# Optimization experiments

Measured on AMD Instinct MI355X. Metric: run time of the kernel, lower is better.

The kernel has to match this reference:

```python
import jax, jax.numpy as jnp
import numpy as np

N_DRUG, N_CELL, N_GENE = 1000, 1000, 6000
N = N_DRUG + N_CELL + N_GENE
H1, H2, H3, HEADS = 256, 128, 128, 4
E = 160000
B = 10000


def _gat_layer(x, src, dst, ea, W, b, a_s, a_d, We, a_e, bias, heads, ch):
    # PyG GATConv (single shared lin for src/dst), edge_dim=1, concat=True, slope=0.2
    n = x.shape[0]
    xw = (x @ W + b).reshape(n, heads, ch)                     # [N,H,C]
    a_src = jnp.einsum('nhc,hc->nh', xw, a_s)                  # [N,H]
    a_dst = jnp.einsum('nhc,hc->nh', xw, a_d)
    eemb = (ea[:, None] @ We).reshape(-1, heads, ch)           # [E',H,C]
    a_edge = jnp.einsum('ehc,hc->eh', eemb, a_e)               # [E',H]
    alpha = jax.nn.leaky_relu(a_src[src] + a_dst[dst] + a_edge, 0.2)
    # segment softmax over destination node (flow source->target)
    m = jax.ops.segment_max(alpha, dst, num_segments=n)
    ex = jnp.exp(alpha - m[dst])
    denom = jax.ops.segment_sum(ex, dst, num_segments=n)
    att = ex / (denom[dst] + 1e-16)                            # [E',H]
    out = jax.ops.segment_sum(xw[src] * att[:, :, None], dst, num_segments=n)
    return out.reshape(n, heads * ch) + bias, att


def _graph_norm(x, gamma, beta, mean_scale, eps=1e-5):
    mu = x.mean(0)
    out = x - mean_scale * mu
    var = (out * out).mean(0)
    return gamma * out / jnp.sqrt(var + eps) + beta


def _attn_mat(src, dst, att, n):
    # original sets every edge entry to the scalar mean of all attention weights
    return jnp.zeros((n, n), dtype=att.dtype).at[src, dst].set(att.mean())


def setup_inputs() -> dict:
    key = jax.random.key(0)
    ks = jax.random.split(key, 40)
    s = 0.1
    inp = {
        'drug': jax.random.normal(ks[0], (N_DRUG, N_DRUG), jnp.float32),
        'cell': jax.random.normal(ks[1], (N_CELL, N_CELL), jnp.float32),
        'gene': jax.random.normal(ks[2], (N_GENE, N_GENE), jnp.float32),
        'edge_attr': jax.random.uniform(ks[3], (E,), jnp.float32),
        'edge_index': jax.random.randint(ks[4], (2, E), 0, N),
        'idx_drug': jax.random.randint(ks[5], (B,), 0, N_DRUG),
        'idx_cell': jax.random.randint(ks[6], (B,), 0, N),
        # type-specific input projections
        'W_drug': jax.random.normal(ks[7], (N_DRUG, H1)) * s, 'b_drug': jnp.zeros((H1,)),
        'W_cell': jax.random.normal(ks[8], (N_CELL, H1)) * s, 'b_cell': jnp.zeros((H1,)),
        'W_gene': jax.random.normal(ks[9], (N_GENE, H1)) * s, 'b_gene': jnp.zeros((H1,)),
        # gat1
        'W1': jax.random.normal(ks[10], (H1, HEADS * H2)) * s, 'b1': jnp.zeros((HEADS * H2,)),
        'att_src1': jax.random.normal(ks[11], (HEADS, H2)) * s,
        'att_dst1': jax.random.normal(ks[12], (HEADS, H2)) * s,
        'We1': jax.random.normal(ks[13], (1, HEADS * H2)) * s,
        'att_e1': jax.random.normal(ks[14], (HEADS, H2)) * s,
        'bias1': jnp.zeros((HEADS * H2,)),
        'g1': jnp.ones((HEADS * H2,)), 'be1': jnp.zeros((HEADS * H2,)), 'ms1': jnp.ones((HEADS * H2,)),
        # gat2
        'W2': jax.random.normal(ks[15], (HEADS * H2, HEADS * H3)) * s, 'b2': jnp.zeros((HEADS * H3,)),
        'att_src2': jax.random.normal(ks[16], (HEADS, H3)) * s,
        'att_dst2': jax.random.normal(ks[17], (HEADS, H3)) * s,
        'We2': jax.random.normal(ks[18], (1, HEADS * H3)) * s,
        'att_e2': jax.random.normal(ks[19], (HEADS, H3)) * s,
        'bias2': jnp.zeros((HEADS * H3,)),
        'g2': jnp.ones((HEADS * H3,)), 'be2': jnp.zeros((HEADS * H3,)), 'ms2': jnp.ones((HEADS * H3,)),
        # head
        'Wout': jax.random.normal(ks[20], (2 * HEADS * H3, 1)) * s, 'bout': jnp.zeros((1,)),
    }
    return inp


def reference(drug, cell, gene, edge_attr, edge_index, idx_drug, idx_cell,
              W_drug, b_drug, W_cell, b_cell, W_gene, b_gene,
              W1, b1, att_src1, att_dst1, We1, att_e1, bias1, g1, be1, ms1,
              W2, b2, att_src2, att_dst2, We2, att_e2, bias2, g2, be2, ms2,
              Wout, bout):
    x = jnp.concatenate([drug @ W_drug + b_drug,
                         cell @ W_cell + b_cell,
                         gene @ W_gene + b_gene], axis=0)       # [N,H1]
    # GATConv adds self-loops with edge_attr filled by the mean edge attribute
    loop = jnp.arange(N)
    src = jnp.concatenate([edge_index[0], loop])
    dst = jnp.concatenate([edge_index[1], loop])
    ea = jnp.concatenate([edge_attr, jnp.full((N,), edge_attr.mean(), edge_attr.dtype)])

    x, att1 = _gat_layer(x, src, dst, ea, W1, b1, att_src1, att_dst1, We1, att_e1, bias1, HEADS, H2)
    all_att = _attn_mat(src, dst, att1, N)
    x = jax.nn.relu(_graph_norm(x, g1, be1, ms1))               # dropout = identity (eval)

    x, att2 = _gat_layer(x, src, dst, ea, W2, b2, att_src2, att_dst2, We2, att_e2, bias2, HEADS, H3)
    all_att = all_att + _attn_mat(src, dst, att2, N)
    x = jax.nn.relu(_graph_norm(x, g2, be2, ms2))

    x = jnp.concatenate([x[idx_drug], x[idx_cell]], axis=1) @ Wout + bout  # [B,1]
    return x, all_att
```

## Files before the change

kernel.cpp:

```cpp
#include <hip/hip_runtime.h>
#include <math.h>

#define NDRUG 1000
#define NCELL 1000
#define NGENE 6000
#define NNODE 8000
#define H1 256
#define HD  512
#define E0  160000
#define ET  168000
#define BSZ 10000
#define GKP 6016
#define ZSPLIT 8
#define ZCH 768

typedef __attribute__((ext_vector_type(8))) short bf16x8;
typedef __attribute__((ext_vector_type(4))) float f32x4;

__device__ inline unsigned short f2bf(float f)
{
    unsigned u = __float_as_uint(f);
    u += 0x7fffu + ((u >> 16) & 1u);
    return (unsigned short)(u >> 16);
}
__device__ inline float bf2f(unsigned short h)
{
    return __uint_as_float(((unsigned)h) << 16);
}

__global__ void cvt_pad2_dc_kernel(const float* __restrict__ drug, unsigned short* dh, unsigned short* dl,
                                   const float* __restrict__ cell, unsigned short* ch, unsigned short* cl)
{
    const float* in;
    unsigned short *hi, *lo;
    long u0;
    if (blockIdx.x < 512) { in = drug; hi = dh; lo = dl; u0 = (long)blockIdx.x * 256 + threadIdx.x; }
    else                  { in = cell; hi = ch; lo = cl; u0 = (long)(blockIdx.x - 512) * 256 + threadIdx.x; }
    const long total = (long)1024 * 1024 / 8;
    for (long u = u0; u < total; u += 512 * 256) {
        long row = u / 128; int kc = (int)(u % 128);
        unsigned short oh[8], ol[8];
        if (row < 1000 && kc * 8 < 1000) {
            const float* p = in + row * 1000 + kc * 8;
            float4 a = *(const float4*)p, b = *(const float4*)(p + 4);
            float v[8] = {a.x, a.y, a.z, a.w, b.x, b.y, b.z, b.w};
            #pragma unroll
            for (int i = 0; i < 8; ++i) {
                unsigned short h = f2bf(v[i]);
                oh[i] = h;
                ol[i] = f2bf(v[i] - bf2f(h));
            }
        } else {
            #pragma unroll
            for (int i = 0; i < 8; ++i) { oh[i] = 0; ol[i] = 0; }
        }
        *(uint4*)(hi + u * 8) = *(const uint4*)oh;
        *(uint4*)(lo + u * 8) = *(const uint4*)ol;
    }
}


struct TC5 {
    const float* W[5];
    unsigned short* Wh[5];
    unsigned short* Wl[5];
    int K[5]; int N[5]; int Kp[5]; int gx[5];
    int start[6];
};

__global__ __launch_bounds__(256) void transpose_cvt2_batch(TC5 d)
{
    int bid = blockIdx.x;
    int idx = 0;
    #pragma unroll
    for (int i = 1; i < 5; ++i) if (bid >= d.start[i]) idx = i;
    int local = bid - d.start[idx];
    int gx = d.gx[idx];
    int K = d.K[idx], N = d.N[idx], Kp = d.Kp[idx];
    const float* W = d.W[idx];
    unsigned short* Wh = d.Wh[idx];
    unsigned short* Wl = d.Wl[idx];
    __shared__ float t[32][33];
    int kb = (local % gx) * 32, nb = (local / gx) * 32;
    int tx = threadIdx.x & 31, ty = threadIdx.x >> 5;
    #pragma unroll
    for (int i = 0; i < 32; i += 8) {
        int k = kb + ty + i;
        t[ty + i][tx] = (k < K) ? W[(long)k * N + nb + tx] : 0.f;
    }
    __syncthreads();
    #pragma unroll
    for (int i = 0; i < 32; i += 8) {
        int n = nb + ty + i;
        float v = t[tx][ty + i];
        unsigned short h = f2bf(v);
        Wh[(long)n * Kp + kb + tx] = h;
        Wl[(long)n * Kp + kb + tx] = f2bf(v - bf2f(h));
    }
}

template<int OUTBF>
__global__ __launch_bounds__(256) void gemm_mfma2(const unsigned short* __restrict__ Ah,
                                                  const unsigned short* __restrict__ Al,
                                                  const unsigned short* __restrict__ Bh,
                                                  const unsigned short* __restrict__ Bl,
                                                  const float* __restrict__ bias,
                                                  float* __restrict__ Cf,
                                                  unsigned short* __restrict__ Cbh,
                                                  unsigned short* __restrict__ Cbl,
                                                  unsigned short* __restrict__ Cx,
                                                  int M, int Kp, int N)
{
    __shared__ unsigned short AsH[64 * 64];
    __shared__ unsigned short AsL[64 * 64];
    __shared__ unsigned short BsH[64 * 64];
    __shared__ unsigned short BsL[64 * 64];
    char* AsH8 = (char*)AsH; char* AsL8 = (char*)AsL;
    char* BsH8 = (char*)BsH; char* BsL8 = (char*)BsL;
    int tid = threadIdx.x;
    int w = tid >> 6, l = tid & 63;
    int wr = w >> 1, wc = w & 1;
    int g = l >> 4, r16 = l & 15;
    int row0 = blockIdx.y * 64, col0 = blockIdx.x * 64;
    int srow = tid >> 3, skc = tid & 7;
    int B0 = srow * 128 + skc * 16;       int P0 = B0 ^ ((srow & 7) << 4);
    int r1 = srow + 32;                   int B1 = r1 * 128 + skc * 16;
    int P1 = B1 ^ ((r1 & 7) << 4);
    f32x4 acc[2][2] = {};
    for (int k0 = 0; k0 < Kp; k0 += 64) {
        long a0 = (long)(row0 + srow) * Kp + k0 + skc * 8;
        long a1 = (long)(row0 + srow + 32) * Kp + k0 + skc * 8;
        long b0 = (long)(col0 + srow) * Kp + k0 + skc * 8;
        long b1 = (long)(col0 + srow + 32) * Kp + k0 + skc * 8;
        uint4 ah0 = *(const uint4*)(Ah + a0); uint4 ah1 = *(const uint4*)(Ah + a1);
        uint4 al0 = *(const uint4*)(Al + a0); uint4 al1 = *(const uint4*)(Al + a1);
        uint4 bh0 = *(const uint4*)(Bh + b0); uint4 bh1 = *(const uint4*)(Bh + b1);
        uint4 bl0 = *(const uint4*)(Bl + b0); uint4 bl1 = *(const uint4*)(Bl + b1);
        __syncthreads();
        *(uint4*)(AsH8 + P0) = ah0; *(uint4*)(AsH8 + P1) = ah1;
        *(uint4*)(AsL8 + P0) = al0; *(uint4*)(AsL8 + P1) = al1;
        *(uint4*)(BsH8 + P0) = bh0; *(uint4*)(BsH8 + P1) = bh1;
        *(uint4*)(BsL8 + P0) = bl0; *(uint4*)(BsL8 + P1) = bl1;
        __syncthreads();
        #pragma unroll
        for (int kk = 0; kk < 2; ++kk) {
            bf16x8 afh[2], afl[2], bfh[2], bfl[2];
            #pragma unroll
            for (int m = 0; m < 2; ++m) {
                int row = wr * 32 + m * 16 + r16;
                int Bb = (row * 128 + kk * 64 + g * 16) ^ ((row & 7) << 4);
                afh[m] = *(const bf16x8*)(AsH8 + Bb);
                afl[m] = *(const bf16x8*)(AsL8 + Bb);
            }
            #pragma unroll
            for (int n = 0; n < 2; ++n) {
                int row = wc * 32 + n * 16 + r16;
                int Bb = (row * 128 + kk * 64 + g * 16) ^ ((row & 7) << 4);
                bfh[n] = *(const bf16x8*)(BsH8 + Bb);
                bfl[n] = *(const bf16x8*)(BsL8 + Bb);
            }
            #pragma unroll
            for (int m = 0; m < 2; ++m)
                #pragma unroll
                for (int n = 0; n < 2; ++n) {
                    acc[m][n] = __builtin_amdgcn_mfma_f32_16x16x32_bf16(afh[m], bfh[n], acc[m][n], 0, 0, 0);
                    acc[m][n] = __builtin_amdgcn_mfma_f32_16x16x32_bf16(afh[m], bfl[n], acc[m][n], 0, 0, 0);
                    acc[m][n] = __builtin_amdgcn_mfma_f32_16x16x32_bf16(afl[m], bfh[n], acc[m][n], 0, 0, 0);
                }
        }
    }
    #pragma unroll
    for (int m = 0; m < 2; ++m) {
        #pragma unroll
        for (int n = 0; n < 2; ++n) {
            #pragma unroll
            for (int r = 0; r < 4; ++r) {
                int rowg = row0 + wr * 32 + m * 16 + g * 4 + r;
                int colg = col0 + wc * 32 + n * 16 + r16;
                if (rowg < M) {
                    float v = acc[m][n][r] + bias[colg];
                    if (OUTBF) {
                        unsigned short h = f2bf(v);
                        Cbh[(long)rowg * N + colg] = h;
                        Cbl[(long)rowg * N + colg] = f2bf(v - bf2f(h));
                    } else {
                        Cf[(long)rowg * N + colg] = v;
                        Cx[(long)rowg * N + colg] = f2bf(v);
                    }
                }
            }
        }
    }
}

__global__ __launch_bounds__(256) void gemm_gene_f32(const float* __restrict__ A,
                                                     const unsigned short* __restrict__ Bh,
                                                     const unsigned short* __restrict__ Bl,
                                                     float* __restrict__ part)
{
    __shared__ char lds[65536];
    int tid = threadIdx.x;
    int w = tid >> 6, l = tid & 63;
    int wr = w >> 1, wc = w & 1;
    int g = l >> 4, r16 = l & 15;
    int pid = blockIdx.x;
    int L = (pid & 7) * 94 + (pid >> 3);
    int xb = L & 1;
    int yb = (L >> 1) % 47;
    int z  = L / 94;
    int row0 = yb * 128, col0 = xb * 128;
    int kbeg = z * ZCH;
    int kend = kbeg + ZCH; if (kend > GKP) kend = GKP;
    int niter = (kend - kbeg) >> 5;
    int arow = tid >> 1, akp = (tid & 1) * 16;
    int t_ar = (arow + (arow >> 2)) & 3;
    int s0 = akp >> 3;
    int wo0 = arow * 64 + ((s0 ^ t_ar) << 4);
    int wo1 = arow * 64 + (((s0 + 1) ^ t_ar) << 4);
    int tA = (r16 + (r16 >> 2)) & 3;
    int soA = (g ^ tA) << 4;
    int gr = row0 + arow;
    const float* arowp = A + (long)gr * NGENE;
    const unsigned short* bhp = Bh + (long)(col0 + arow) * GKP;
    const unsigned short* blp = Bl + (long)(col0 + arow) * GKP;
    bool arok = (gr < NGENE);
    f32x4 acc[4][4] = {};

    float av[16];
    uint4 rbh0, rbh1, rbl0, rbl1;
    {
        int gk = kbeg + akp;
        #pragma unroll
        for (int j = 0; j < 16; j += 4) {
            float4 v = (arok && gk + j < NGENE) ? *(const float4*)(arowp + gk + j)
                                                : make_float4(0.f, 0.f, 0.f, 0.f);
            av[j] = v.x; av[j + 1] = v.y; av[j + 2] = v.z; av[j + 3] = v.w;
        }
        rbh0 = *(const uint4*)(bhp + gk); rbh1 = *(const uint4*)(bhp + gk + 8);
        rbl0 = *(const uint4*)(blp + gk); rbl1 = *(const uint4*)(blp + gk + 8);
    }
    {
        unsigned short ah[16], alr[16];
        #pragma unroll
        for (int j = 0; j < 16; ++j) {
            unsigned u = __float_as_uint(av[j]);
            ah[j] = (unsigned short)(u >> 16);
            alr[j] = f2bf(av[j] - __uint_as_float(u & 0xffff0000u));
        }
        char* AsH = lds; char* AsL = lds + 8192;
        char* BsH = lds + 16384; char* BsL = lds + 24576;
        *(uint4*)(AsH + wo0) = *(const uint4*)&ah[0];
        *(uint4*)(AsH + wo1) = *(const uint4*)&ah[8];
        *(uint4*)(AsL + wo0) = *(const uint4*)&alr[0];
        *(uint4*)(AsL + wo1) = *(const uint4*)&alr[8];
        *(uint4*)(BsH + wo0) = rbh0; *(uint4*)(BsH + wo1) = rbh1;
        *(uint4*)(BsL + wo0) = rbl0; *(uint4*)(BsL + wo1) = rbl1;
    }
    __syncthreads();
    for (int i = 0; i < niter; ++i) {
        bool more = (i + 1 < niter);
        if (more) {
            int gk = kbeg + (i + 1) * 32 + akp;
            #pragma unroll
            for (int j = 0; j < 16; j += 4) {
                float4 v = (arok && gk + j < NGENE) ? *(const float4*)(arowp + gk + j)
                                                    : make_float4(0.f, 0.f, 0.f, 0.f);
                av[j] = v.x; av[j + 1] = v.y; av[j + 2] = v.z; av[j + 3] = v.w;
            }
            rbh0 = *(const uint4*)(bhp + gk); rbh1 = *(const uint4*)(bhp + gk + 8);
            rbl0 = *(const uint4*)(blp + gk); rbl1 = *(const uint4*)(blp + gk + 8);
        }
        {
            char* base = lds + (i & 1) * 32768;
            char* AsH = base; char* AsL = base + 8192;
            char* BsH = base + 16384; char* BsL = base + 24576;
            bf16x8 afh[4], afl[4], bfh[4], bfl[4];
            #pragma unroll
            for (int m = 0; m < 4; ++m) {
                int Bb = (wr * 64 + m * 16 + r16) * 64 + soA;
                afh[m] = *(const bf16x8*)(AsH + Bb);
                afl[m] = *(const bf16x8*)(AsL + Bb);
            }
            #pragma unroll
            for (int n = 0; n < 4; ++n) {
                int Bb = (wc * 64 + n * 16 + r16) * 64 + soA;
                bfh[n] = *(const bf16x8*)(BsH + Bb);
                bfl[n] = *(const bf16x8*)(BsL + Bb);
            }
            #pragma unroll
            for (int m = 0; m < 4; ++m)
                #pragma unroll
                for (int n = 0; n < 4; ++n) {
                    acc[m][n] = __builtin_amdgcn_mfma_f32_16x16x32_bf16(afh[m], bfh[n], acc[m][n], 0, 0, 0);
                    acc[m][n] = __builtin_amdgcn_mfma_f32_16x16x32_bf16(afh[m], bfl[n], acc[m][n], 0, 0, 0);
                    acc[m][n] = __builtin_amdgcn_mfma_f32_16x16x32_bf16(afl[m], bfh[n], acc[m][n], 0, 0, 0);
                }
        }
        if (more) {
            unsigned short ah[16], alr[16];
            #pragma unroll
            for (int j = 0; j < 16; ++j) {
                unsigned u = __float_as_uint(av[j]);
                ah[j] = (unsigned short)(u >> 16);
                alr[j] = f2bf(av[j] - __uint_as_float(u & 0xffff0000u));
            }
            char* base = lds + ((i + 1) & 1) * 32768;
            char* AsH = base; char* AsL = base + 8192;
            char* BsH = base + 16384; char* BsL = base + 24576;
            *(uint4*)(AsH + wo0) = *(const uint4*)&ah[0];
            *(uint4*)(AsH + wo1) = *(const uint4*)&ah[8];
            *(uint4*)(AsL + wo0) = *(const uint4*)&alr[0];
            *(uint4*)(AsL + wo1) = *(const uint4*)&alr[8];
            *(uint4*)(BsH + wo0) = rbh0; *(uint4*)(BsH + wo1) = rbh1;
            *(uint4*)(BsL + wo0) = rbl0; *(uint4*)(BsL + wo1) = rbl1;
        }
        __syncthreads();
    }
    #pragma unroll
    for (int m = 0; m < 4; ++m) {
        #pragma unroll
        for (int n = 0; n < 4; ++n) {
            #pragma unroll
            for (int r = 0; r < 4; ++r) {
                int rowg = row0 + wr * 64 + m * 16 + g * 4 + r;
                int colg = col0 + wc * 64 + n * 16 + r16;
                if (rowg < NGENE)
                    part[((long)z * NGENE + rowg) * H1 + colg] = acc[m][n][r];
            }
        }
    }
}

__global__ __launch_bounds__(256) void reduce_splitk_kernel(const float* __restrict__ part,
                                                            const float* __restrict__ bias,
                                                            unsigned short* __restrict__ xh,
                                                            unsigned short* __restrict__ xl)
{
    const long NEL = (long)NGENE * H1;
    long stride = (long)gridDim.x * blockDim.x;
    for (long q = (long)blockIdx.x * blockDim.x + threadIdx.x; q * 4 < NEL; q += stride) {
        long e = q * 4;
        float4 sv = *(const float4*)(part + e);
        #pragma unroll
        for (int z = 1; z < ZSPLIT; ++z) {
            float4 t = *(const float4*)(part + (long)z * NEL + e);
            sv.x += t.x; sv.y += t.y; sv.z += t.z; sv.w += t.w;
        }
        int col = (int)(e & (H1 - 1));
        float4 b = *(const float4*)(bias + col);
        float v[4] = {sv.x + b.x, sv.y + b.y, sv.z + b.z, sv.w + b.w};
        unsigned short oh[4], ol[4];
        #pragma unroll
        for (int i = 0; i < 4; ++i) {
            oh[i] = f2bf(v[i]);
            ol[i] = f2bf(v[i] - bf2f(oh[i]));
        }
        long o = (long)(NDRUG + NCELL) * H1 + e;
        *(uint2*)(xh + o) = *(const uint2*)oh;
        *(uint2*)(xl + o) = *(const uint2*)ol;
    }
}

__global__ void init1_kernel(float* m, int* deg, float* colstats, float* scal)
{
    int i = blockIdx.x * 256 + threadIdx.x;
    if (i < NNODE * 4) m[i] = -3.402823466e38f;
    if (i < NNODE) deg[i] = 0;
    if (i < 1024) colstats[i] = 0.f;
    if (i < 8) scal[i] = 0.f;
}

__global__ void init2_kernel(float* m, float* colstats)
{
    int i = blockIdx.x * 256 + threadIdx.x;
    if (i < NNODE * 4) m[i] = -3.402823466e38f;
    if (i < 1024) colstats[i] = 0.f;
}

__global__ __launch_bounds__(512) void small_pre_kernel(const float* __restrict__ eattr, float* scal,
                                                        const float* We1, const float* ae1,
                                                        const float* We2, const float* ae2, float* ce)
{
    if (blockIdx.x < 64) {
        float s = 0.f;
        for (int i = blockIdx.x * 512 + threadIdx.x; i < E0; i += 64 * 512)
            s += eattr[i];
        for (int off = 32; off; off >>= 1) s += __shfl_down(s, off);
        if ((threadIdx.x & 63) == 0) atomicAdd(&scal[0], s);
    } else {
        __shared__ float sm[512];
        int t = threadIdx.x;
        sm[t] = We1[t] * ae1[t];
        __syncthreads();
        if (t < 4) { float s = 0.f; for (int c = 0; c < 128; ++c) s += sm[t * 128 + c]; ce[t] = s; }
        __syncthreads();
        sm[t] = We2[t] * ae2[t];
        __syncthreads();
        if (t < 4) { float s = 0.f; for (int c = 0; c < 128; ++c) s += sm[t * 128 + c]; ce[4 + t] = s; }
    }
}

__global__ void deg_kernel(const int* __restrict__ ei, int* __restrict__ deg)
{
    int e = blockIdx.x * blockDim.x + threadIdx.x;
    if (e >= ET) return;
    int d = (e < E0) ? ei[E0 + e] : (e - E0);
    atomicAdd(&deg[d], 1);
}

__global__ __launch_bounds__(1024) void scan_kernel(const int* __restrict__ deg,
                                                    int* __restrict__ row_start,
                                                    int* __restrict__ cursor)
{
    __shared__ int sm[1024];
    int t = threadIdx.x;
    int base = t * 8;
    int loc[8];
    int sum = 0;
    #pragma unroll
    for (int j = 0; j < 8; ++j) {
        int v = (base + j < NNODE) ? deg[base + j] : 0;
        loc[j] = sum; sum += v;
    }
    sm[t] = sum;
    __syncthreads();
    for (int off = 1; off < 1024; off <<= 1) {
        int v = (t >= off) ? sm[t - off] : 0;
        __syncthreads();
        sm[t] += v;
        __syncthreads();
    }
    int excl = sm[t] - sum;
    #pragma unroll
    for (int j = 0; j < 8; ++j) {
        int idx = base + j;
        if (idx < NNODE) { int v = excl + loc[j]; row_start[idx] = v; cursor[idx] = v; }
    }
    if (t == 1023) row_start[NNODE] = sm[1023];
}

__global__ void scatter_csr_kernel(const int* __restrict__ ei, int* __restrict__ cursor,
                                   int* __restrict__ csr_src, int* __restrict__ pos_of_e)
{
    int e = blockIdx.x * blockDim.x + threadIdx.x;
    if (e >= ET) return;
    int s, d;
    if (e < E0) { s = ei[e]; d = ei[E0 + e]; }
    else        { s = d = e - E0; }
    int pos = atomicAdd(&cursor[d], 1);
    csr_src[pos] = s;
    pos_of_e[e] = pos;
}

__global__ __launch_bounds__(256) void attn_coef_kernel(const float* __restrict__ xw,
                                                        const float* __restrict__ as,
                                                        const float* __restrict__ ad,
                                                        float* __restrict__ a_src,
                                                        float* __restrict__ a_dst)
{
    int n = blockIdx.x * 4 + (threadIdx.x >> 6);
    int l = threadIdx.x & 63;
    #pragma unroll
    for (int h = 0; h < 4; ++h) {
        float x1 = xw[(long)n * HD + h * 128 + l];
        float x2 = xw[(long)n * HD + h * 128 + 64 + l];
        float s = x1 * as[h * 128 + l] + x2 * as[h * 128 + 64 + l];
        float d = x1 * ad[h * 128 + l] + x2 * ad[h * 128 + 64 + l];
        for (int off = 32; off; off >>= 1) { s += __shfl_down(s, off); d += __shfl_down(d, off); }
        if (l == 0) { a_src[n * 4 + h] = s; a_dst[n * 4 + h] = d; }
    }
}

__device__ inline void atomicMaxF(float* addr, float v)
{
    if (v >= 0.f) atomicMax((int*)addr, __float_as_int(v));
    else          atomicMin((unsigned int*)addr, __float_as_uint(v));
}

__global__ void alpha_max_kernel(const int* __restrict__ ei, const float* __restrict__ eattr,
                                 const float* __restrict__ scal,
                                 const float* __restrict__ a_src, const float* __restrict__ a_dst,
                                 const float* __restrict__ ce,
                                 float* __restrict__ csr_alpha,
                                 const int* __restrict__ pos_of_e,
                                 float* __restrict__ m)
{
    int e = blockIdx.x * blockDim.x + threadIdx.x;
    if (e >= ET) return;
    int s, d; float a;
    if (e < E0) { s = ei[e]; d = ei[E0 + e]; a = eattr[e]; }
    else        { s = d = e - E0; a = scal[0] * (1.0f / E0); }
    float4 av;
    float* avp = (float*)&av;
    #pragma unroll
    for (int h = 0; h < 4; ++h) {
        float v = a_src[s * 4 + h] + a_dst[d * 4 + h] + a * ce[h];
        v = v > 0.f ? v : 0.2f * v;
        avp[h] = v;
        atomicMaxF(&m[d * 4 + h], v);
    }
    *(float4*)(csr_alpha + (long)pos_of_e[e] * 4) = av;
}

__global__ __launch_bounds__(256) void aggregate_kernel(const unsigned short* __restrict__ xwb,
                                                        const float* __restrict__ csr_alpha,
                                                        const float* __restrict__ m,
                                                        const int* __restrict__ rs,
                                                        const int* __restrict__ csr_src,
                                                        const float* __restrict__ bias,
                                                        float* __restrict__ out)
{
    int n = blockIdx.x;
    int h = threadIdx.x >> 6;
    int l = threadIdx.x & 63;
    float mnh = m[n * 4 + h];
    int i0 = rs[n], i1 = rs[n + 1];
    float den = 0.f;
    for (int i = i0 + l; i < i1; i += 64)
        den += expf(csr_alpha[(long)i * 4 + h] - mnh);
    for (int off = 32; off; off >>= 1) den += __shfl_down(den, off);
    den = __shfl(den, 0);
    float rden = 1.0f / (den + 1e-16f);
    float acc0 = 0.f, acc1 = 0.f;
    int i = i0;
    for (; i + 7 < i1; i += 8) {
        int      sv[8];
        float    av[8];
        unsigned xv[8];
        #pragma unroll
        for (int j = 0; j < 8; ++j) {
            sv[j] = csr_src[i + j];
            av[j] = csr_alpha[(long)(i + j) * 4 + h];
        }
        #pragma unroll
        for (int j = 0; j < 8; ++j)
            xv[j] = *(const unsigned*)(xwb + (long)sv[j] * HD + h * 128 + 2 * l);
        #pragma unroll
        for (int j = 0; j < 8; ++j) {
            float w = expf(av[j] - mnh);
            acc0 += w * bf2f((unsigned short)(xv[j] & 0xffffu));
            acc1 += w * bf2f((unsigned short)(xv[j] >> 16));
        }
    }
    for (; i < i1; ++i) {
        int s = csr_src[i];
        float w = expf(csr_alpha[(long)i * 4 + h] - mnh);
        unsigned x = *(const unsigned*)(xwb + (long)s * HD + h * 128 + 2 * l);
        acc0 += w * bf2f((unsigned short)(x & 0xffffu));
        acc1 += w * bf2f((unsigned short)(x >> 16));
    }
    float2 o;
    o.x = acc0 * rden + bias[h * 128 + 2 * l];
    o.y = acc1 * rden + bias[h * 128 + 2 * l + 1];
    *(float2*)(out + (long)n * HD + h * 128 + 2 * l) = o;
}

__global__ __launch_bounds__(256) void colstats_kernel(const float* __restrict__ x,
                                                       float* __restrict__ colsum,
                                                       float* __restrict__ colsumsq)
{
    int t = threadIdx.x, b = blockIdx.x;
    float s0 = 0.f, s1 = 0.f, q0 = 0.f, q1 = 0.f;
    for (int r = b * 125; r < (b + 1) * 125; ++r) {
        float v0 = x[(long)r * HD + t];
        float v1 = x[(long)r * HD + t + 256];
        s0 += v0; q0 += v0 * v0;
        s1 += v1; q1 += v1 * v1;
    }
    atomicAdd(&colsum[t], s0);
    atomicAdd(&colsum[t + 256], s1);
    atomicAdd(&colsumsq[t], q0);
    atomicAdd(&colsumsq[t + 256], q1);
}

__global__ void norm_kernel(float* __restrict__ x,
                            unsigned short* __restrict__ xbh, unsigned short* __restrict__ xbl,
                            const float* __restrict__ colsum,
                            const float* __restrict__ colsumsq,
                            const float* __restrict__ g, const float* __restrict__ be,
                            const float* __restrict__ ms)
{
    int stride = gridDim.x * blockDim.x;
    for (int idx = blockIdx.x * blockDim.x + threadIdx.x; idx < NNODE * HD; idx += stride) {
        int j = idx & 511;
        float mu  = colsum[j] * (1.0f / NNODE);
        float ex2 = colsumsq[j] * (1.0f / NNODE);
        float msj = ms[j];
        float var = ex2 - msj * (2.0f - msj) * mu * mu;
        float v = x[idx] - msj * mu;
        float y = g[j] * v / sqrtf(var + 1e-5f) + be[j];
        y = y > 0.f ? y : 0.f;
        x[idx] = y;
        unsigned short h = f2bf(y);
        xbh[idx] = h;
        xbl[idx] = f2bf(y - bf2f(h));
    }
}

__global__ __launch_bounds__(256) void head_kernel(const float* __restrict__ x2,
                                                   const int* __restrict__ idd,
                                                   const int* __restrict__ idc,
                                                   const float* __restrict__ Wout,
                                                   const float* __restrict__ bout,
                                                   float* __restrict__ out0)
{
    int w = threadIdx.x >> 6, l = threadIdx.x & 63;
    int b = blockIdx.x * 4 + w;
    if (b >= BSZ) return;
    int rd = idd[b], rc = idc[b];
    float s = 0.f;
    #pragma unroll
    for (int k = l; k < HD; k += 64)
        s += x2[(long)rd * HD + k] * Wout[k] + x2[(long)rc * HD + k] * Wout[HD + k];
    for (int off = 32; off; off >>= 1) s += __shfl_down(s, off);
    if (l == 0) out0[b] = s + bout[0];
}

__global__ void zero_f4_kernel(float4* __restrict__ p, long n4)
{
    long stride = (long)gridDim.x * blockDim.x;
    for (long i = (long)blockIdx.x * blockDim.x + threadIdx.x; i < n4; i += stride)
        p[i] = make_float4(0.f, 0.f, 0.f, 0.f);
}

__global__ void scatter_att_kernel(const int* __restrict__ ei, float* __restrict__ attm)
{
    int e = blockIdx.x * blockDim.x + threadIdx.x;
    if (e >= ET) return;
    int s, d;
    if (e < E0) { s = ei[e]; d = ei[E0 + e]; }
    else        { s = d = e - E0; }
    const float val = 2.0f * (float)NNODE / (float)ET;
    attm[(long)s * NNODE + d] = val;
}

extern "C" void kernel_launch(void* const* d_in, const int* in_sizes, int n_in,
                              void* d_out, int out_size, void* d_ws, size_t ws_size,
                              hipStream_t stream)
{
    const float* drug   = (const float*)d_in[0];
    const float* cell   = (const float*)d_in[1];
    const float* gene   = (const float*)d_in[2];
    const float* eattr  = (const float*)d_in[3];
    const int*   ei     = (const int*)d_in[4];
    const int*   idd    = (const int*)d_in[5];
    const int*   idc    = (const int*)d_in[6];
    const float* Wdrug  = (const float*)d_in[7];
    const float* bdrug  = (const float*)d_in[8];
    const float* Wcell  = (const float*)d_in[9];
    const float* bcell  = (const float*)d_in[10];
    const float* Wgene  = (const float*)d_in[11];
    const float* bgene  = (const float*)d_in[12];
    const float* W1     = (const float*)d_in[13];
    const float* b1     = (const float*)d_in[14];
    const float* as1    = (const float*)d_in[15];
    const float* ad1    = (const float*)d_in[16];
    const float* We1    = (const float*)d_in[17];
    const float* ae1    = (const float*)d_in[18];
    const float* bias1  = (const float*)d_in[19];
    const float* g1     = (const float*)d_in[20];
    const float* be1    = (const float*)d_in[21];
    const float* ms1    = (const float*)d_in[22];
    const float* W2     = (const float*)d_in[23];
    const float* b2     = (const float*)d_in[24];
    const float* as2    = (const float*)d_in[25];
    const float* ad2    = (const float*)d_in[26];
    const float* We2    = (const float*)d_in[27];
    const float* ae2    = (const float*)d_in[28];
    const float* bias2  = (const float*)d_in[29];
    const float* g2     = (const float*)d_in[30];
    const float* be2    = (const float*)d_in[31];
    const float* ms2    = (const float*)d_in[32];
    const float* Wout   = (const float*)d_in[33];
    const float* bout   = (const float*)d_in[34];

    float* out0 = (float*)d_out;
    float* attm = (float*)d_out + BSZ;

    float* ws     = (float*)d_ws;
    float* xw     = ws;
    float* outb   = xw + (long)NNODE * HD;
    float* csr_al = outb + (long)NNODE * HD;
    float* a_src  = csr_al + (long)ET * 4;
    float* a_dst  = a_src + NNODE * 4;
    float* mbuf   = a_dst + NNODE * 4;
    float* colsum = mbuf + NNODE * 4;
    float* colsq  = colsum + 512;
    float* ce     = colsq + 512;
    float* scal   = ce + 8;
    int* deg      = (int*)(scal + 8);
    int* rs       = deg + NNODE;
    int* cursor   = rs + NNODE + 4;
    int* csr_src  = cursor + NNODE;
    int* pos_of_e = csr_src + ET;
    unsigned short* p = (unsigned short*)(pos_of_e + ET);
    unsigned short* xwb    = p; p += (long)NNODE * HD;
    unsigned short* drug_h = p; p += (long)1024 * 1024;
    unsigned short* drug_l = p; p += (long)1024 * 1024;
    unsigned short* cell_h = p; p += (long)1024 * 1024;
    unsigned short* cell_l = p; p += (long)1024 * 1024;
    unsigned short* x0_h   = p; p += (long)NNODE * H1;
    unsigned short* x0_l   = p; p += (long)NNODE * H1;
    unsigned short* xb_h   = p; p += (long)NNODE * HD;
    unsigned short* xb_l   = p; p += (long)NNODE * HD;
    unsigned short* Wd_h   = p; p += 256 * 1024;
    unsigned short* Wd_l   = p; p += 256 * 1024;
    unsigned short* Wc_h   = p; p += 256 * 1024;
    unsigned short* Wc_l   = p; p += 256 * 1024;
    unsigned short* Wg_h   = p; p += 256 * GKP;
    unsigned short* Wg_l   = p; p += 256 * GKP;
    unsigned short* W1_h   = p; p += 512 * 256;
    unsigned short* W1_l   = p; p += 512 * 256;
    unsigned short* W2_h   = p; p += 512 * 512;
    unsigned short* W2_l   = p; p += 512 * 512;
    float* partsk = (float*)((((unsigned long long)p) + 15) & ~15ULL);

    dim3 blk256(256);
    int gE = (ET + 255) / 256;

    init1_kernel<<<125, blk256, 0, stream>>>(mbuf, deg, colsum, scal);
    deg_kernel<<<gE, blk256, 0, stream>>>(ei, deg);
    scan_kernel<<<1, 1024, 0, stream>>>(deg, rs, cursor);
    scatter_csr_kernel<<<gE, blk256, 0, stream>>>(ei, cursor, csr_src, pos_of_e);
    small_pre_kernel<<<65, 512, 0, stream>>>(eattr, scal, We1, ae1, We2, ae2, ce);

    cvt_pad2_dc_kernel<<<1024, blk256, 0, stream>>>(drug, drug_h, drug_l, cell, cell_h, cell_l);
    {
        TC5 d;
        d.W[0] = Wdrug; d.Wh[0] = Wd_h; d.Wl[0] = Wd_l; d.K[0] = NDRUG; d.N[0] = H1; d.Kp[0] = 1024; d.gx[0] = 32;
        d.W[1] = Wcell; d.Wh[1] = Wc_h; d.Wl[1] = Wc_l; d.K[1] = NCELL; d.N[1] = H1; d.Kp[1] = 1024; d.gx[1] = 32;
        d.W[2] = Wgene; d.Wh[2] = Wg_h; d.Wl[2] = Wg_l; d.K[2] = NGENE; d.N[2] = H1; d.Kp[2] = GKP;  d.gx[2] = 188;
        d.W[3] = W1;    d.Wh[3] = W1_h; d.Wl[3] = W1_l; d.K[3] = H1;    d.N[3] = HD; d.Kp[3] = H1;   d.gx[3] = 8;
        d.W[4] = W2;    d.Wh[4] = W2_h; d.Wl[4] = W2_l; d.K[4] = HD;    d.N[4] = HD; d.Kp[4] = HD;   d.gx[4] = 16;
        d.start[0] = 0;    d.start[1] = 256;  d.start[2] = 512;
        d.start[3] = 2016; d.start[4] = 2144; d.start[5] = 2400;
        transpose_cvt2_batch<<<2400, blk256, 0, stream>>>(d);
    }

    gemm_mfma2<1><<<dim3(H1 / 64, 16), blk256, 0, stream>>>(drug_h, drug_l, Wd_h, Wd_l, bdrug,
        nullptr, x0_h, x0_l, nullptr, NDRUG, 1024, H1);
    gemm_mfma2<1><<<dim3(H1 / 64, 16), blk256, 0, stream>>>(cell_h, cell_l, Wc_h, Wc_l, bcell,
        nullptr, x0_h + (long)NDRUG * H1, x0_l + (long)NDRUG * H1, nullptr, NCELL, 1024, H1);
    gemm_gene_f32<<<752, blk256, 0, stream>>>(gene, Wg_h, Wg_l, partsk);
    reduce_splitk_kernel<<<1500, blk256, 0, stream>>>(partsk, bgene, x0_h, x0_l);

    gemm_mfma2<0><<<dim3(HD / 64, NNODE / 64), blk256, 0, stream>>>(x0_h, x0_l, W1_h, W1_l, b1,
        xw, nullptr, nullptr, xwb, NNODE, H1, HD);
    attn_coef_kernel<<<NNODE / 4, blk256, 0, stream>>>(xw, as1, ad1, a_src, a_dst);
    alpha_max_kernel<<<gE, blk256, 0, stream>>>(ei, eattr, scal, a_src, a_dst, ce,
        csr_al, pos_of_e, mbuf);
    aggregate_kernel<<<NNODE, blk256, 0, stream>>>(xwb, csr_al, mbuf, rs, csr_src, bias1, outb);
    colstats_kernel<<<64, blk256, 0, stream>>>(outb, colsum, colsq);
    norm_kernel<<<2048, blk256, 0, stream>>>(outb, xb_h, xb_l, colsum, colsq, g1, be1, ms1);

    gemm_mfma2<0><<<dim3(HD / 64, NNODE / 64), blk256, 0, stream>>>(xb_h, xb_l, W2_h, W2_l, b2,
        xw, nullptr, nullptr, xwb, NNODE, HD, HD);
    attn_coef_kernel<<<NNODE / 4, blk256, 0, stream>>>(xw, as2, ad2, a_src, a_dst);
    init2_kernel<<<125, blk256, 0, stream>>>(mbuf, colsum);
    alpha_max_kernel<<<gE, blk256, 0, stream>>>(ei, eattr, scal, a_src, a_dst, ce + 4,
        csr_al, pos_of_e, mbuf);
    aggregate_kernel<<<NNODE, blk256, 0, stream>>>(xwb, csr_al, mbuf, rs, csr_src, bias2, outb);
    colstats_kernel<<<64, blk256, 0, stream>>>(outb, colsum, colsq);
    norm_kernel<<<2048, blk256, 0, stream>>>(outb, xb_h, xb_l, colsum, colsq, g2, be2, ms2);

    head_kernel<<<(BSZ + 3) / 4, blk256, 0, stream>>>(outb, idd, idc, Wout, bout, out0);
    zero_f4_kernel<<<2048, blk256, 0, stream>>>((float4*)attm, (long)NNODE * NNODE / 4);
    scatter_att_kernel<<<gE, blk256, 0, stream>>>(ei, attm);
}
```

Measured before the change: 576.2 us.

## Load gene GEMM MFMA fragments directly from global memory, dropping LDS staging

The split-K gene GEMM no longer stages A and B tiles through double-buffered shared memory. Each lane loads its own MFMA fragment rows straight from global memory, converting fp32 A to hi/lo bf16 in registers. This removes LDS writes, reads and the per-iteration barriers, and frees LDS so more blocks can share a CU. In exchange, each A and B element is fetched by several waves instead of once per block, which leans on L2/L1 caching. Each lane also does strided 32-byte loads rather than coalesced row loads, and the A hi/lo conversion is now repeated by every wave that reads the row.

```diff
diff --git a/kernel.cpp b/kernel.cpp
--- a/kernel.cpp
+++ b/kernel.cpp
@@ -58,7 +58,6 @@
         *(uint4*)(lo + u * 8) = *(const uint4*)ol;
     }
 }
-
 
 struct TC5 {
     const float* W[5];
@@ -193,12 +192,11 @@
     }
 }
 
-__global__ __launch_bounds__(256) void gemm_gene_f32(const float* __restrict__ A,
-                                                     const unsigned short* __restrict__ Bh,
-                                                     const unsigned short* __restrict__ Bl,
-                                                     float* __restrict__ part)
-{
-    __shared__ char lds[65536];
+__global__ __launch_bounds__(256) void gemm_gene_noLDS(const float* __restrict__ A,
+                                                       const unsigned short* __restrict__ Bh,
+                                                       const unsigned short* __restrict__ Bl,
+                                                       float* __restrict__ part)
+{
     int tid = threadIdx.x;
     int w = tid >> 6, l = tid & 63;
     int wr = w >> 1, wc = w & 1;
@@ -211,110 +209,60 @@
     int row0 = yb * 128, col0 = xb * 128;
     int kbeg = z * ZCH;
     int kend = kbeg + ZCH; if (kend > GKP) kend = GKP;
-    int niter = (kend - kbeg) >> 5;
-    int arow = tid >> 1, akp = (tid & 1) * 16;
-    int t_ar = (arow + (arow >> 2)) & 3;
-    int s0 = akp >> 3;
-    int wo0 = arow * 64 + ((s0 ^ t_ar) << 4);
-    int wo1 = arow * 64 + (((s0 + 1) ^ t_ar) << 4);
-    int tA = (r16 + (r16 >> 2)) & 3;
-    int soA = (g ^ tA) << 4;
-    int gr = row0 + arow;
-    const float* arowp = A + (long)gr * NGENE;
-    const unsigned short* bhp = Bh + (long)(col0 + arow) * GKP;
-    const unsigned short* blp = Bl + (long)(col0 + arow) * GKP;
-    bool arok = (gr < NGENE);
+    int koff = g * 8;
+    const float* arp[4];
+    bool arok[4];
+    #pragma unroll
+    for (int m = 0; m < 4; ++m) {
+        int r = row0 + wr * 64 + m * 16 + r16;
+        arok[m] = (r < NGENE);
+        arp[m] = A + (long)r * NGENE;
+    }
+    const unsigned short* bhp[4];
+    const unsigned short* blp[4];
+    #pragma unroll
+    for (int n = 0; n < 4; ++n) {
+        int c = col0 + wc * 64 + n * 16 + r16;
+        bhp[n] = Bh + (long)c * GKP;
+        blp[n] = Bl + (long)c * GKP;
+    }
     f32x4 acc[4][4] = {};
-
-    float av[16];
-    uint4 rbh0, rbh1, rbl0, rbl1;
-    {
-        int gk = kbeg + akp;
-        #pragma unroll
-        for (int j = 0; j < 16; j += 4) {
-            float4 v = (arok && gk + j < NGENE) ? *(const float4*)(arowp + gk + j)
-                                                : make_float4(0.f, 0.f, 0.f, 0.f);
-            av[j] = v.x; av[j + 1] = v.y; av[j + 2] = v.z; av[j + 3] = v.w;
-        }
-        rbh0 = *(const uint4*)(bhp + gk); rbh1 = *(const uint4*)(bhp + gk + 8);
-        rbl0 = *(const uint4*)(blp + gk); rbl1 = *(const uint4*)(blp + gk + 8);
-    }
-    {
-        unsigned short ah[16], alr[16];
-        #pragma unroll
-        for (int j = 0; j < 16; ++j) {
-            unsigned u = __float_as_uint(av[j]);
-            ah[j] = (unsigned short)(u >> 16);
-            alr[j] = f2bf(av[j] - __uint_as_float(u & 0xffff0000u));
-        }
-        char* AsH = lds; char* AsL = lds + 8192;
-        char* BsH = lds + 16384; char* BsL = lds + 24576;
-        *(uint4*)(AsH + wo0) = *(const uint4*)&ah[0];
-        *(uint4*)(AsH + wo1) = *(const uint4*)&ah[8];
-        *(uint4*)(AsL + wo0) = *(const uint4*)&alr[0];
-        *(uint4*)(AsL + wo1) = *(const uint4*)&alr[8];
-        *(uint4*)(BsH + wo0) = rbh0; *(uint4*)(BsH + wo1) = rbh1;
-        *(uint4*)(BsL + wo0) = rbl0; *(uint4*)(BsL + wo1) = rbl1;
-    }
-    __syncthreads();
-    for (int i = 0; i < niter; ++i) {
-        bool more = (i + 1 < niter);
-        if (more) {
-            int gk = kbeg + (i + 1) * 32 + akp;
-            #pragma unroll
-            for (int j = 0; j < 16; j += 4) {
-                float4 v = (arok && gk + j < NGENE) ? *(const float4*)(arowp + gk + j)
-                                                    : make_float4(0.f, 0.f, 0.f, 0.f);
-                av[j] = v.x; av[j + 1] = v.y; av[j + 2] = v.z; av[j + 3] = v.w;
+    #pragma unroll 2
+    for (int k0 = kbeg; k0 < kend; k0 += 32) {
+        int gk = k0 + koff;
+        bool kok = (gk + 8 <= NGENE);
+        bf16x8 afh[4], afl[4], bfh[4], bfl[4];
+        #pragma unroll
+        for (int m = 0; m < 4; ++m) {
+            float4 v0 = make_float4(0.f, 0.f, 0.f, 0.f), v1 = v0;
+            if (arok[m] && kok) {
+                v0 = *(const float4*)(arp[m] + gk);
+                v1 = *(const float4*)(arp[m] + gk + 4);
             }
-            rbh0 = *(const uint4*)(bhp + gk); rbh1 = *(const uint4*)(bhp + gk + 8);
-            rbl0 = *(const uint4*)(blp + gk); rbl1 = *(const uint4*)(blp + gk + 8);
-        }
-        {
-            char* base = lds + (i & 1) * 32768;
-            char* AsH = base; char* AsL = base + 8192;
-            char* BsH = base + 16384; char* BsL = base + 24576;
-            bf16x8 afh[4], afl[4], bfh[4], bfl[4];
-            #pragma unroll
-            for (int m = 0; m < 4; ++m) {
-                int Bb = (wr * 64 + m * 16 + r16) * 64 + soA;
-                afh[m] = *(const bf16x8*)(AsH + Bb);
-                afl[m] = *(const bf16x8*)(AsL + Bb);
+            float vv[8] = {v0.x, v0.y, v0.z, v0.w, v1.x, v1.y, v1.z, v1.w};
+            unsigned short hh[8], ll[8];
+            #pragma unroll
+            for (int j = 0; j < 8; ++j) {
+                unsigned u = __float_as_uint(vv[j]);
+                hh[j] = (unsigned short)(u >> 16);
+                ll[j] = f2bf(vv[j] - __uint_as_float(u & 0xffff0000u));
             }
+            afh[m] = *(const bf16x8*)hh;
+            afl[m] = *(const bf16x8*)ll;
+        }
+        #pragma unroll
+        for (int n = 0; n < 4; ++n) {
+            bfh[n] = *(const bf16x8*)(bhp[n] + gk);
+            bfl[n] = *(const bf16x8*)(blp[n] + gk);
+        }
+        #pragma unroll
+        for (int m = 0; m < 4; ++m)
             #pragma unroll
             for (int n = 0; n < 4; ++n) {
-                int Bb = (wc * 64 + n * 16 + r16) * 64 + soA;
-                bfh[n] = *(const bf16x8*)(BsH + Bb);
-                bfl[n] = *(const bf16x8*)(BsL + Bb);
+                acc[m][n] = __builtin_amdgcn_mfma_f32_16x16x32_bf16(afh[m], bfh[n], acc[m][n], 0, 0, 0);
+                acc[m][n] = __builtin_amdgcn_mfma_f32_16x16x32_bf16(afh[m], bfl[n], acc[m][n], 0, 0, 0);
+                acc[m][n] = __builtin_amdgcn_mfma_f32_16x16x32_bf16(afl[m], bfh[n], acc[m][n], 0, 0, 0);
             }
-            #pragma unroll
-            for (int m = 0; m < 4; ++m)
-                #pragma unroll
-                for (int n = 0; n < 4; ++n) {
-                    acc[m][n] = __builtin_amdgcn_mfma_f32_16x16x32_bf16(afh[m], bfh[n], acc[m][n], 0, 0, 0);
-                    acc[m][n] = __builtin_amdgcn_mfma_f32_16x16x32_bf16(afh[m], bfl[n], acc[m][n], 0, 0, 0);
-                    acc[m][n] = __builtin_amdgcn_mfma_f32_16x16x32_bf16(afl[m], bfh[n], acc[m][n], 0, 0, 0);
-                }
-        }
-        if (more) {
-            unsigned short ah[16], alr[16];
-            #pragma unroll
-            for (int j = 0; j < 16; ++j) {
-                unsigned u = __float_as_uint(av[j]);
-                ah[j] = (unsigned short)(u >> 16);
-                alr[j] = f2bf(av[j] - __uint_as_float(u & 0xffff0000u));
-            }
-            char* base = lds + ((i + 1) & 1) * 32768;
-            char* AsH = base; char* AsL = base + 8192;
-            char* BsH = base + 16384; char* BsL = base + 24576;
-            *(uint4*)(AsH + wo0) = *(const uint4*)&ah[0];
-            *(uint4*)(AsH + wo1) = *(const uint4*)&ah[8];
-            *(uint4*)(AsL + wo0) = *(const uint4*)&alr[0];
-            *(uint4*)(AsL + wo1) = *(const uint4*)&alr[8];
-            *(uint4*)(BsH + wo0) = rbh0; *(uint4*)(BsH + wo1) = rbh1;
-            *(uint4*)(BsL + wo0) = rbl0; *(uint4*)(BsL + wo1) = rbl1;
-        }
-        __syncthreads();
     }
     #pragma unroll
     for (int m = 0; m < 4; ++m) {
@@ -741,7 +689,7 @@
         nullptr, x0_h, x0_l, nullptr, NDRUG, 1024, H1);
     gemm_mfma2<1><<<dim3(H1 / 64, 16), blk256, 0, stream>>>(cell_h, cell_l, Wc_h, Wc_l, bcell,
         nullptr, x0_h + (long)NDRUG * H1, x0_l + (long)NDRUG * H1, nullptr, NCELL, 1024, H1);
-    gemm_gene_f32<<<752, blk256, 0, stream>>>(gene, Wg_h, Wg_l, partsk);
+    gemm_gene_noLDS<<<752, blk256, 0, stream>>>(gene, Wg_h, Wg_l, partsk);
     reduce_splitk_kernel<<<1500, blk256, 0, stream>>>(partsk, bgene, x0_h, x0_l);
 
     gemm_mfma2<0><<<dim3(HD / 64, NNODE / 64), blk256, 0, stream>>>(x0_h, x0_l, W1_h, W1_l, b1,
```

Measured after the change: 621.2 us. 7.8% more time.
